# Optimization experiments

Hardware: AMD Instinct MI355X
Metric: run time of the kernel (lower is better)

Reference implementation:

```python
import jax, jax.numpy as jnp
import numpy as np

UNITARY_SIZE = 128  # 2**7, gate acts on 7 qubits
N_QUBITS = 23
GATE_IDCS = [[0,1,2,3,4,5,6],[7,8,9,10,11,12,13],[3,5,7,9,11,13,15],[16,17,18,19,20,21,22]]


def setup_inputs() -> dict:
    key = jax.random.key(0)
    k1, k2 = jax.random.split(key)
    state = jax.random.normal(k1, (2, 2 ** N_QUBITS), dtype=jnp.float32)
    U = jax.random.normal(k2, (len(GATE_IDCS), 2, UNITARY_SIZE, UNITARY_SIZE), dtype=jnp.float32)
    return {"state": state, "U": U}


def _apply_gate(state, Ur, Ui, idcs, n):
    # permutation exactly as in run_circuit: targeted qubits to the front,
    # leading real/imag channel (dim 0) kept in place
    perm = [0] + [q + 1 for q in idcs + [q for q in range(n) if q not in idcs]]
    inv_perm = np.argsort(np.array(perm)).tolist()
    s = state.reshape((2,) + (2,) * n)
    s = jnp.transpose(s, perm)
    s = s.reshape(2, -1, UNITARY_SIZE)  # (channel, M, 128); matmul contracts last dim
    sr, si = s[0], s[1]
    # Karatsuba 3-matmul complex multiply, as in the NKI kernel
    Wr = jnp.einsum('ka,ma->mk', Ur, sr)
    Wi = jnp.einsum('ka,ma->mk', Ui, si)
    SASB = jnp.einsum('ka,ma->mk', Ur + Ui, sr + si)
    real = Wr - Wi
    imag = SASB - Wr - Wi
    # Faithful to the kernel: it stores the imag result into channel 0 and the
    # real result into channel 1 (swapped relative to the input convention).
    s = jnp.stack([imag, real], axis=0)
    s = s.reshape((2,) + (2,) * n)
    s = jnp.transpose(s, inv_perm)
    return s.reshape(2, -1)


def reference(state, U):
    for g, idcs in enumerate(GATE_IDCS):
        state = _apply_gate(state, U[g, 0], U[g, 1], idcs, N_QUBITS)
    return state
```

## Files before the change

kernel.cpp:

```cpp
#include <hip/hip_runtime.h>


typedef __attribute__((ext_vector_type(8))) short bf16x8;
typedef __attribute__((ext_vector_type(4))) short bf16x4;
typedef __attribute__((ext_vector_type(4))) float f32x4;

static constexpr int NSTATE = 1 << 23;

__device__ inline void tsplit(float x, unsigned short& h, unsigned short& l) {
    unsigned int u = __float_as_uint(x);
    h = (unsigned short)(u >> 16);
    float hf = __uint_as_float(u & 0xFFFF0000u);
    l = (unsigned short)(__float_as_uint(x - hf) >> 16);
}

__device__ inline void split8(const float* xv, bf16x8& hv, bf16x8& lv) {
    #pragma unroll
    for (int i = 0; i < 8; ++i) {
        unsigned short h, l;
        tsplit(xv[i], h, l);
        hv[i] = (short)h; lv[i] = (short)l;
    }
}

__device__ inline void rsplit(float x, unsigned short& h, unsigned short& l) {
    unsigned int u = __float_as_uint(x);
    unsigned int r = (u + 0x7FFFu + ((u >> 16) & 1u)) >> 16;
    h = (unsigned short)r;
    float hf = __uint_as_float(r << 16);
    unsigned int u2 = __float_as_uint(x - hf);
    l = (unsigned short)((u2 + 0x7FFFu + ((u2 >> 16) & 1u)) >> 16);
}

__device__ inline float wElem(const float* __restrict__ Ug, int kp, int ap) {
    const int co = kp >> 7, ci = ap >> 7;
    const float v = Ug[((co == ci) ? 16384 : 0) + (kp & 127) * 128 + (ap & 127)];
    return (co & ci) ? -v : v;
}

__device__ inline int fragOff(int i, int t) {
    const int frag = (i >> 4) * 8 + (t >> 5);
    const int slot = (i & 15) + 16 * ((t >> 3) & 3);
    return frag * 512 + slot * 8 + (t & 7);
}

__device__ inline int slotSwz(int frag, int slot) {
    return slot ^ ((slot >> 3) & 6) ^ (frag & 7);
}

__device__ inline void dma16(const float* gp, float* lp) {
    __builtin_amdgcn_global_load_lds(
        (const __attribute__((address_space(1))) unsigned int*)gp,
        (__attribute__((address_space(3))) unsigned int*)lp,
        16, 0, 0);
}

__global__ __launch_bounds__(256)
void prep_all(const float* __restrict__ U,
              unsigned short* __restrict__ WAh, unsigned short* __restrict__ WAl,
              unsigned short* __restrict__ WBh, unsigned short* __restrict__ WBl) {
    __shared__ float Arow[256];
    const int t = threadIdx.x;
    if (blockIdx.x < 256) {
        const int i = blockIdx.x;
        Arow[t] = wElem(U + 2 * 32768, i, t);
        __syncthreads();
        float r = 0.f;
        #pragma unroll 8
        for (int k = 0; k < 256; ++k)
            r = fmaf(Arow[k], wElem(U + 32768, k, t), r);
        __syncthreads();
        Arow[t] = r;
        __syncthreads();
        float s = 0.f;
        #pragma unroll 8
        for (int k = 0; k < 256; ++k)
            s = fmaf(Arow[k], wElem(U, k, t), s);
        unsigned short h, l;
        rsplit(s, h, l);
        const int off = fragOff(i, t);
        WAh[off] = h; WAl[off] = l;
    } else {
        const int i = blockIdx.x - 256;
        unsigned short h, l;
        rsplit(wElem(U + 3 * 32768, i, t), h, l);
        const int off = fragOff(i, t);
        WBh[off] = h; WBl[off] = l;
    }
}

__global__ __launch_bounds__(1024, 4)
void fused6(const float* __restrict__ src, float* __restrict__ dst,
            const unsigned short* __restrict__ WAh, const unsigned short* __restrict__ WAl,
            const unsigned short* __restrict__ WBh, const unsigned short* __restrict__ WBl)
{
    __shared__ unsigned short S[65536];
    float* Sf            = (float*)S;
    unsigned short* Mh   = S;
    unsigned short* Ml   = S + 32768;

    const int t    = threadIdx.x;
    const int lane = t & 63;
    const int w    = t >> 6;
    const int col  = lane & 15, quad = lane >> 4;
    const int mg   = w & 3;
    const int ng   = w >> 2;
    const size_t hbase = (size_t)blockIdx.x * 16384;

    #pragma unroll
    for (int j = 0; j < 4; ++j) {
        const int r0 = w * 8 + (j & 3) * 2;
        const int r  = r0 + (lane >> 5);
        const int cb = ((lane & 31) << 4) ^ ((r & 7) << 4);
        dma16(src + hbase + (size_t)r * 128 + (cb >> 2), Sf + r0 * 128);
    }
    __syncthreads();
    #pragma unroll
    for (int j = 4; j < 8; ++j) {
        const int r0 = 128 + w * 8 + (j & 3) * 2;
        const int r  = r0 + (lane >> 5);
        const int cb = ((lane & 31) << 4) ^ ((r & 7) << 4);
        dma16(src + (size_t)NSTATE + hbase + (size_t)(r & 127) * 128 + (cb >> 2),
              Sf + r0 * 128);
    }

    f32x4 acc[2][4];
    #pragma unroll
    for (int mi = 0; mi < 2; ++mi)
        #pragma unroll
        for (int nj = 0; nj < 4; ++nj) acc[mi][nj] = (f32x4)0.f;

    #pragma unroll
    for (int ks = 0; ks < 8; ++ks) {
        if (ks == 4) __syncthreads();
        const int ch  = ks >> 2;
        const int cb0 = (ks & 3) * 128 + quad * 32;
        bf16x8 ah[2], al[2];
        #pragma unroll
        for (int mi = 0; mi < 2; ++mi) {
            const int r   = ch * 128 + (mg * 2 + mi) * 16 + col;
            const int swz = (r & 7) << 4;
            const char* rowp = (const char*)Sf + r * 512;
            float xv[8];
            *(float4*)&xv[0] = *(const float4*)(rowp + (cb0 ^ swz));
            *(float4*)&xv[4] = *(const float4*)(rowp + ((cb0 + 16) ^ swz));
            split8(xv, ah[mi], al[mi]);
        }
        bf16x8 bh[4], bl[4];
        #pragma unroll
        for (int nj = 0; nj < 4; ++nj) {
            const int fo = ((ng * 4 + nj) * 8 + ks) * 512 + lane * 8;
            bh[nj] = *(const bf16x8*)(WAh + fo);
            bl[nj] = *(const bf16x8*)(WAl + fo);
        }
        #pragma unroll
        for (int nj = 0; nj < 4; ++nj)
            #pragma unroll
            for (int mi = 0; mi < 2; ++mi)
                acc[mi][nj] = __builtin_amdgcn_mfma_f32_16x16x32_bf16(ah[mi], bh[nj], acc[mi][nj], 0, 0, 0);
        #pragma unroll
        for (int nj = 0; nj < 4; ++nj)
            #pragma unroll
            for (int mi = 0; mi < 2; ++mi)
                acc[mi][nj] = __builtin_amdgcn_mfma_f32_16x16x32_bf16(al[mi], bh[nj], acc[mi][nj], 0, 0, 0);
        #pragma unroll
        for (int nj = 0; nj < 4; ++nj)
            #pragma unroll
            for (int mi = 0; mi < 2; ++mi)
                acc[mi][nj] = __builtin_amdgcn_mfma_f32_16x16x32_bf16(ah[mi], bl[nj], acc[mi][nj], 0, 0, 0);
    }
    __syncthreads();

    #pragma unroll
    for (int mi = 0; mi < 2; ++mi) {
        const int mt  = mg * 2 + mi;
        const int oct = (mt * 2 + (quad >> 1)) & 3;
        #pragma unroll
        for (int nj = 0; nj < 4; ++nj) {
            const int nt    = ng * 4 + nj;
            const int frag2 = (nt & 7) * 8 + (nt >> 3) * 4 + (mt >> 1);
            const int slot2 = col + 16 * oct;
            const int soff  = frag2 * 512 + slotSwz(frag2, slot2) * 8 + (quad & 1) * 4;
            unsigned short hhs[4], lls[4];
            #pragma unroll
            for (int r = 0; r < 4; ++r) tsplit(acc[mi][nj][r], hhs[r], lls[r]);
            bf16x4 hv = { (short)hhs[0], (short)hhs[1], (short)hhs[2], (short)hhs[3] };
            bf16x4 lv = { (short)lls[0], (short)lls[1], (short)lls[2], (short)lls[3] };
            *(bf16x4*)&Mh[soff] = hv;
            *(bf16x4*)&Ml[soff] = lv;
        }
    }
    __syncthreads();

    f32x4 acc2[2][4];
    #pragma unroll
    for (int mi = 0; mi < 2; ++mi)
        #pragma unroll
        for (int nj = 0; nj < 4; ++nj) acc2[mi][nj] = (f32x4)0.f;

    #pragma unroll
    for (int ks2 = 0; ks2 < 8; ++ks2) {
        bf16x8 a2h[2], a2l[2];
        #pragma unroll
        for (int mi = 0; mi < 2; ++mi) {
            const int fr = (mg * 2 + mi) * 8 + ks2;
            const int fo = fr * 512 + slotSwz(fr, lane) * 8;
            a2h[mi] = *(const bf16x8*)&Mh[fo];
            a2l[mi] = *(const bf16x8*)&Ml[fo];
        }
        bf16x8 bh2[4], bl2[4];
        #pragma unroll
        for (int nj = 0; nj < 4; ++nj) {
            const int fo = ((ng * 4 + nj) * 8 + ks2) * 512 + lane * 8;
            bh2[nj] = *(const bf16x8*)(WBh + fo);
            bl2[nj] = *(const bf16x8*)(WBl + fo);
        }
        #pragma unroll
        for (int nj = 0; nj < 4; ++nj)
            #pragma unroll
            for (int mi = 0; mi < 2; ++mi)
                acc2[mi][nj] = __builtin_amdgcn_mfma_f32_16x16x32_bf16(a2h[mi], bh2[nj], acc2[mi][nj], 0, 0, 0);
        #pragma unroll
        for (int nj = 0; nj < 4; ++nj)
            #pragma unroll
            for (int mi = 0; mi < 2; ++mi)
                acc2[mi][nj] = __builtin_amdgcn_mfma_f32_16x16x32_bf16(a2l[mi], bh2[nj], acc2[mi][nj], 0, 0, 0);
        #pragma unroll
        for (int nj = 0; nj < 4; ++nj)
            #pragma unroll
            for (int mi = 0; mi < 2; ++mi)
                acc2[mi][nj] = __builtin_amdgcn_mfma_f32_16x16x32_bf16(a2h[mi], bl2[nj], acc2[mi][nj], 0, 0, 0);
    }

    #pragma unroll
    for (int nj = 0; nj < 4; ++nj) {
        const int kp2  = (ng * 4 + nj) * 16 + col;
        const int chpp = kp2 >> 7, kb = kp2 & 127;
        float* o = dst + (size_t)chpp * NSTATE + hbase + (size_t)kb * 128;
        #pragma unroll
        for (int mi = 0; mi < 2; ++mi) {
            const int ka = (mg * 2 + mi) * 16 + quad * 4;
            *(float4*)(o + ka) = *(float4*)&acc2[mi][nj];
        }
    }
}

extern "C" void kernel_launch(void* const* d_in, const int* in_sizes, int n_in,
                              void* d_out, int out_size, void* d_ws, size_t ws_size,
                              hipStream_t stream) {
    const float* state = (const float*)d_in[0];
    const float* U     = (const float*)d_in[1];
    float* out = (float*)d_out;

    unsigned short* WAh = (unsigned short*)d_ws;
    unsigned short* WAl = WAh + 65536;
    unsigned short* WBh = WAh + 2 * 65536;
    unsigned short* WBl = WAh + 3 * 65536;

    prep_all<<<512, 256, 0, stream>>>(U, WAh, WAl, WBh, WBl);
    fused6 <<<512, 1024, 0, stream>>>(state, out, WAh, WAl, WBh, WBl);
}
```

Measured before the change: 167.5 us.

## Split fused kernel into two kernels with intermediate staged through global output

Splits the single fused kernel into midK, which computes the first matmul and writes the bf16 hi/lo split intermediate into the output buffer, and outK, which reads it back and computes the second matmul. Block size drops from 1024 to 512 threads, and each wave's tile grows from 2x4 to 4x4 MFMA fragments for more register reuse. LDS use falls to 64KB of floats in midK and none in outK. The cost is an extra global round trip for the intermediate plus a second launch, and outK reads and overwrites the same dst region in place, relying on the __syncthreads before the stores.

```diff
diff --git a/kernel.cpp b/kernel.cpp
--- a/kernel.cpp
+++ b/kernel.cpp
@@ -42,10 +42,6 @@
     const int frag = (i >> 4) * 8 + (t >> 5);
     const int slot = (i & 15) + 16 * ((t >> 3) & 3);
     return frag * 512 + slot * 8 + (t & 7);
-}
-
-__device__ inline int slotSwz(int frag, int slot) {
-    return slot ^ ((slot >> 3) & 6) ^ (frag & 7);
 }
 
 __device__ inline void dma16(const float* gp, float* lp) {
@@ -89,148 +85,144 @@
     }
 }
 
-__global__ __launch_bounds__(1024, 4)
-void fused6(const float* __restrict__ src, float* __restrict__ dst,
-            const unsigned short* __restrict__ WAh, const unsigned short* __restrict__ WAl,
-            const unsigned short* __restrict__ WBh, const unsigned short* __restrict__ WBl)
+__global__ __launch_bounds__(512, 4)
+void midK(const float* __restrict__ src, float* __restrict__ dst,
+          const unsigned short* __restrict__ WAh, const unsigned short* __restrict__ WAl)
 {
-    __shared__ unsigned short S[65536];
-    float* Sf            = (float*)S;
-    unsigned short* Mh   = S;
-    unsigned short* Ml   = S + 32768;
+    __shared__ float Sf[16384];
 
     const int t    = threadIdx.x;
     const int lane = t & 63;
     const int w    = t >> 6;
     const int col  = lane & 15, quad = lane >> 4;
-    const int mg   = w & 3;
-    const int ng   = w >> 2;
+    const int mg   = w & 1;
+    const int ng   = w >> 1;
     const size_t hbase = (size_t)blockIdx.x * 16384;
 
-    #pragma unroll
-    for (int j = 0; j < 4; ++j) {
-        const int r0 = w * 8 + (j & 3) * 2;
-        const int r  = r0 + (lane >> 5);
-        const int cb = ((lane & 31) << 4) ^ ((r & 7) << 4);
-        dma16(src + hbase + (size_t)r * 128 + (cb >> 2), Sf + r0 * 128);
-    }
-    __syncthreads();
-    #pragma unroll
-    for (int j = 4; j < 8; ++j) {
-        const int r0 = 128 + w * 8 + (j & 3) * 2;
-        const int r  = r0 + (lane >> 5);
-        const int cb = ((lane & 31) << 4) ^ ((r & 7) << 4);
-        dma16(src + (size_t)NSTATE + hbase + (size_t)(r & 127) * 128 + (cb >> 2),
-              Sf + r0 * 128);
-    }
-
-    f32x4 acc[2][4];
-    #pragma unroll
-    for (int mi = 0; mi < 2; ++mi)
+    unsigned short* MhG = (unsigned short*)(dst + hbase);
+    unsigned short* MlG = (unsigned short*)(dst + (size_t)NSTATE + hbase);
+
+    f32x4 acc[4][4];
+    #pragma unroll
+    for (int mi = 0; mi < 4; ++mi)
         #pragma unroll
         for (int nj = 0; nj < 4; ++nj) acc[mi][nj] = (f32x4)0.f;
 
     #pragma unroll
-    for (int ks = 0; ks < 8; ++ks) {
-        if (ks == 4) __syncthreads();
-        const int ch  = ks >> 2;
-        const int cb0 = (ks & 3) * 128 + quad * 32;
-        bf16x8 ah[2], al[2];
-        #pragma unroll
-        for (int mi = 0; mi < 2; ++mi) {
-            const int r   = ch * 128 + (mg * 2 + mi) * 16 + col;
-            const int swz = (r & 7) << 4;
-            const char* rowp = (const char*)Sf + r * 512;
-            float xv[8];
-            *(float4*)&xv[0] = *(const float4*)(rowp + (cb0 ^ swz));
-            *(float4*)&xv[4] = *(const float4*)(rowp + ((cb0 + 16) ^ swz));
-            split8(xv, ah[mi], al[mi]);
-        }
+    for (int half = 0; half < 2; ++half) {
+        if (half) __syncthreads();
+        #pragma unroll
+        for (int j = 0; j < 8; ++j) {
+            const int r0 = w * 16 + j * 2;
+            const int r  = r0 + (lane >> 5);
+            const int cb = ((lane & 31) << 4) ^ ((r & 7) << 4);
+            dma16(src + (size_t)half * NSTATE + hbase + (size_t)r * 128 + (cb >> 2),
+                  Sf + r0 * 128);
+        }
+        __syncthreads();
+
+        #pragma unroll
+        for (int ks4 = 0; ks4 < 4; ++ks4) {
+            const int ks = half * 4 + ks4;
+            bf16x8 bh[4], bl[4];
+            #pragma unroll
+            for (int nj = 0; nj < 4; ++nj) {
+                const int fo = ((ng * 4 + nj) * 8 + ks) * 512 + lane * 8;
+                bh[nj] = *(const bf16x8*)(WAh + fo);
+                bl[nj] = *(const bf16x8*)(WAl + fo);
+            }
+            const int cb0 = ks4 * 128 + quad * 32;
+            #pragma unroll
+            for (int mi = 0; mi < 4; ++mi) {
+                const int r   = (mg * 4 + mi) * 16 + col;
+                const int swz = (r & 7) << 4;
+                const char* rowp = (const char*)Sf + r * 512;
+                float xv[8];
+                *(float4*)&xv[0] = *(const float4*)(rowp + (cb0 ^ swz));
+                *(float4*)&xv[4] = *(const float4*)(rowp + ((cb0 + 16) ^ swz));
+                bf16x8 ah, al;
+                split8(xv, ah, al);
+                #pragma unroll
+                for (int nj = 0; nj < 4; ++nj)
+                    acc[mi][nj] = __builtin_amdgcn_mfma_f32_16x16x32_bf16(ah, bh[nj], acc[mi][nj], 0, 0, 0);
+                #pragma unroll
+                for (int nj = 0; nj < 4; ++nj)
+                    acc[mi][nj] = __builtin_amdgcn_mfma_f32_16x16x32_bf16(al, bh[nj], acc[mi][nj], 0, 0, 0);
+                #pragma unroll
+                for (int nj = 0; nj < 4; ++nj)
+                    acc[mi][nj] = __builtin_amdgcn_mfma_f32_16x16x32_bf16(ah, bl[nj], acc[mi][nj], 0, 0, 0);
+            }
+        }
+    }
+
+    #pragma unroll
+    for (int mi = 0; mi < 4; ++mi) {
+        const int mt  = mg * 4 + mi;
+        const int oct = (mt * 2 + (quad >> 1)) & 3;
+        #pragma unroll
+        for (int nj = 0; nj < 4; ++nj) {
+            const int nt   = ng * 4 + nj;
+            const int frag = (nt & 7) * 8 + (nt >> 3) * 4 + (mt >> 1);
+            const int soff = frag * 512 + (col + 16 * oct) * 8 + (quad & 1) * 4;
+            unsigned short hh[4], ll[4];
+            #pragma unroll
+            for (int r = 0; r < 4; ++r) tsplit(acc[mi][nj][r], hh[r], ll[r]);
+            bf16x4 hv = { (short)hh[0], (short)hh[1], (short)hh[2], (short)hh[3] };
+            bf16x4 lv = { (short)ll[0], (short)ll[1], (short)ll[2], (short)ll[3] };
+            *(bf16x4*)(MhG + soff) = hv;
+            *(bf16x4*)(MlG + soff) = lv;
+        }
+    }
+}
+
+__global__ __launch_bounds__(512, 4)
+void outK(float* __restrict__ dst,
+          const unsigned short* __restrict__ WBh, const unsigned short* __restrict__ WBl)
+{
+    const int t    = threadIdx.x;
+    const int lane = t & 63;
+    const int w    = t >> 6;
+    const int col  = lane & 15, quad = lane >> 4;
+    const int mg   = w & 1;
+    const int ng   = w >> 1;
+    const size_t hbase = (size_t)blockIdx.x * 16384;
+
+    const unsigned short* MhG = (const unsigned short*)(dst + hbase);
+    const unsigned short* MlG = (const unsigned short*)(dst + (size_t)NSTATE + hbase);
+
+    f32x4 acc2[4][4];
+    #pragma unroll
+    for (int mi = 0; mi < 4; ++mi)
+        #pragma unroll
+        for (int nj = 0; nj < 4; ++nj) acc2[mi][nj] = (f32x4)0.f;
+
+    #pragma unroll
+    for (int ks2 = 0; ks2 < 8; ++ks2) {
         bf16x8 bh[4], bl[4];
-        #pragma unroll
-        for (int nj = 0; nj < 4; ++nj) {
-            const int fo = ((ng * 4 + nj) * 8 + ks) * 512 + lane * 8;
-            bh[nj] = *(const bf16x8*)(WAh + fo);
-            bl[nj] = *(const bf16x8*)(WAl + fo);
-        }
-        #pragma unroll
-        for (int nj = 0; nj < 4; ++nj)
-            #pragma unroll
-            for (int mi = 0; mi < 2; ++mi)
-                acc[mi][nj] = __builtin_amdgcn_mfma_f32_16x16x32_bf16(ah[mi], bh[nj], acc[mi][nj], 0, 0, 0);
-        #pragma unroll
-        for (int nj = 0; nj < 4; ++nj)
-            #pragma unroll
-            for (int mi = 0; mi < 2; ++mi)
-                acc[mi][nj] = __builtin_amdgcn_mfma_f32_16x16x32_bf16(al[mi], bh[nj], acc[mi][nj], 0, 0, 0);
-        #pragma unroll
-        for (int nj = 0; nj < 4; ++nj)
-            #pragma unroll
-            for (int mi = 0; mi < 2; ++mi)
-                acc[mi][nj] = __builtin_amdgcn_mfma_f32_16x16x32_bf16(ah[mi], bl[nj], acc[mi][nj], 0, 0, 0);
-    }
-    __syncthreads();
-
-    #pragma unroll
-    for (int mi = 0; mi < 2; ++mi) {
-        const int mt  = mg * 2 + mi;
-        const int oct = (mt * 2 + (quad >> 1)) & 3;
-        #pragma unroll
-        for (int nj = 0; nj < 4; ++nj) {
-            const int nt    = ng * 4 + nj;
-            const int frag2 = (nt & 7) * 8 + (nt >> 3) * 4 + (mt >> 1);
-            const int slot2 = col + 16 * oct;
-            const int soff  = frag2 * 512 + slotSwz(frag2, slot2) * 8 + (quad & 1) * 4;
-            unsigned short hhs[4], lls[4];
-            #pragma unroll
-            for (int r = 0; r < 4; ++r) tsplit(acc[mi][nj][r], hhs[r], lls[r]);
-            bf16x4 hv = { (short)hhs[0], (short)hhs[1], (short)hhs[2], (short)hhs[3] };
-            bf16x4 lv = { (short)lls[0], (short)lls[1], (short)lls[2], (short)lls[3] };
-            *(bf16x4*)&Mh[soff] = hv;
-            *(bf16x4*)&Ml[soff] = lv;
-        }
-    }
-    __syncthreads();
-
-    f32x4 acc2[2][4];
-    #pragma unroll
-    for (int mi = 0; mi < 2; ++mi)
-        #pragma unroll
-        for (int nj = 0; nj < 4; ++nj) acc2[mi][nj] = (f32x4)0.f;
-
-    #pragma unroll
-    for (int ks2 = 0; ks2 < 8; ++ks2) {
-        bf16x8 a2h[2], a2l[2];
-        #pragma unroll
-        for (int mi = 0; mi < 2; ++mi) {
-            const int fr = (mg * 2 + mi) * 8 + ks2;
-            const int fo = fr * 512 + slotSwz(fr, lane) * 8;
-            a2h[mi] = *(const bf16x8*)&Mh[fo];
-            a2l[mi] = *(const bf16x8*)&Ml[fo];
-        }
-        bf16x8 bh2[4], bl2[4];
         #pragma unroll
         for (int nj = 0; nj < 4; ++nj) {
             const int fo = ((ng * 4 + nj) * 8 + ks2) * 512 + lane * 8;
-            bh2[nj] = *(const bf16x8*)(WBh + fo);
-            bl2[nj] = *(const bf16x8*)(WBl + fo);
-        }
-        #pragma unroll
-        for (int nj = 0; nj < 4; ++nj)
-            #pragma unroll
-            for (int mi = 0; mi < 2; ++mi)
-                acc2[mi][nj] = __builtin_amdgcn_mfma_f32_16x16x32_bf16(a2h[mi], bh2[nj], acc2[mi][nj], 0, 0, 0);
-        #pragma unroll
-        for (int nj = 0; nj < 4; ++nj)
-            #pragma unroll
-            for (int mi = 0; mi < 2; ++mi)
-                acc2[mi][nj] = __builtin_amdgcn_mfma_f32_16x16x32_bf16(a2l[mi], bh2[nj], acc2[mi][nj], 0, 0, 0);
-        #pragma unroll
-        for (int nj = 0; nj < 4; ++nj)
-            #pragma unroll
-            for (int mi = 0; mi < 2; ++mi)
-                acc2[mi][nj] = __builtin_amdgcn_mfma_f32_16x16x32_bf16(a2h[mi], bl2[nj], acc2[mi][nj], 0, 0, 0);
-    }
+            bh[nj] = *(const bf16x8*)(WBh + fo);
+            bl[nj] = *(const bf16x8*)(WBl + fo);
+        }
+        #pragma unroll
+        for (int mi = 0; mi < 4; ++mi) {
+            const int fo = ((mg * 4 + mi) * 8 + ks2) * 512 + lane * 8;
+            const bf16x8 a2h = *(const bf16x8*)(MhG + fo);
+            const bf16x8 a2l = *(const bf16x8*)(MlG + fo);
+            #pragma unroll
+            for (int nj = 0; nj < 4; ++nj)
+                acc2[mi][nj] = __builtin_amdgcn_mfma_f32_16x16x32_bf16(a2h, bh[nj], acc2[mi][nj], 0, 0, 0);
+            #pragma unroll
+            for (int nj = 0; nj < 4; ++nj)
+                acc2[mi][nj] = __builtin_amdgcn_mfma_f32_16x16x32_bf16(a2l, bh[nj], acc2[mi][nj], 0, 0, 0);
+            #pragma unroll
+            for (int nj = 0; nj < 4; ++nj)
+                acc2[mi][nj] = __builtin_amdgcn_mfma_f32_16x16x32_bf16(a2h, bl[nj], acc2[mi][nj], 0, 0, 0);
+        }
+    }
+
+    __syncthreads();
 
     #pragma unroll
     for (int nj = 0; nj < 4; ++nj) {
@@ -238,8 +230,8 @@
         const int chpp = kp2 >> 7, kb = kp2 & 127;
         float* o = dst + (size_t)chpp * NSTATE + hbase + (size_t)kb * 128;
         #pragma unroll
-        for (int mi = 0; mi < 2; ++mi) {
-            const int ka = (mg * 2 + mi) * 16 + quad * 4;
+        for (int mi = 0; mi < 4; ++mi) {
+            const int ka = (mg * 4 + mi) * 16 + quad * 4;
             *(float4*)(o + ka) = *(float4*)&acc2[mi][nj];
         }
     }
@@ -258,5 +250,6 @@
     unsigned short* WBl = WAh + 3 * 65536;
 
     prep_all<<<512, 256, 0, stream>>>(U, WAh, WAl, WBh, WBl);
-    fused6 <<<512, 1024, 0, stream>>>(state, out, WAh, WAl, WBh, WBl);
-}
+    midK<<<512, 512, 0, stream>>>(state, out, WAh, WAl);
+    outK<<<512, 512, 0, stream>>>(out, WBh, WBl);
+}
```

Result: slower. 199.2 us (+18.9%).
